# Kernel optimization log

Hardware: AMD Instinct MI355X
Metric: run time of the kernel (lower is better)

## Reference

```python
import jax, jax.numpy as jnp
import numpy as np

EPS = 0.01  # diffusion sampling noise scale


def gru_last(x, Wx, Wh, bx, bh):
    """Run a single-layer GRU (torch gate conventions) over x: [B, L, C] -> final hidden [B, H]."""
    B, L, C = x.shape
    H = Wh.shape[0]
    xg = jnp.einsum('blc,cg->blg', x, Wx) + bx  # precomputed input gates [B, L, 3H]

    def step(h, xg_t):
        hg = h @ Wh + bh
        xr, xz, xn = jnp.split(xg_t, 3, axis=-1)
        hr, hz, hn = jnp.split(hg, 3, axis=-1)
        r = jax.nn.sigmoid(xr + hr)
        z = jax.nn.sigmoid(xz + hz)
        n = jnp.tanh(xn + r * hn)
        h_new = (1.0 - z) * n + z * h
        return h_new, None

    h0 = jnp.zeros((B, H), x.dtype)
    h, _ = jax.lax.scan(step, h0, jnp.swapaxes(xg, 0, 1))
    return h


def gru_aggr(x, Wx, Wh, bx, bh, Wo, bo):
    return gru_last(x, Wx, Wh, bx, bh) @ Wo + bo


def setup_inputs() -> dict:
    key = jax.random.key(0)
    N, C, DEG, H, C_OUT, T = 8000, 64, 16, 128, 64, 4
    ks = jax.random.split(key, 16)

    def lin(k, fan_in, shape):
        return jax.random.normal(k, shape, dtype=jnp.float32) / np.sqrt(fan_in)

    inp = {
        'node_attr': jax.random.normal(ks[0], (N, C), dtype=jnp.float32),
        'neighbors': jax.random.randint(ks[1], (N, DEG), 0, N, dtype=jnp.int32),
        'noise': jax.random.normal(ks[2], (T, N, DEG), dtype=jnp.float32),
        # diff_aggr GRU + output head (edge log-prob comes from channel 0)
        'dWx': lin(ks[3], C, (C, 3 * H)),
        'dWh': lin(ks[4], H, (H, 3 * H)),
        'dbx': jnp.zeros((3 * H,), jnp.float32),
        'dbh': jnp.zeros((3 * H,), jnp.float32),
        'dWo': lin(ks[5], H, (H, C_OUT)),
        'dbo': jnp.zeros((C_OUT,), jnp.float32),
        # walk_aggr GRU + output head (node embedding)
        'wWx': lin(ks[6], C, (C, 3 * H)),
        'wWh': lin(ks[7], H, (H, 3 * H)),
        'wbx': jnp.zeros((3 * H,), jnp.float32),
        'wbh': jnp.zeros((3 * H,), jnp.float32),
        'wWo': lin(ks[8], H, (H, C_OUT)),
        'wbo': jnp.zeros((C_OUT,), jnp.float32),
    }
    return inp


def reference(node_attr, neighbors, noise,
              dWx, dWh, dbx, dbh, dWo, dbo,
              wWx, wWh, wbx, wbh, wWo, wbo):
    N, C = node_attr.shape
    DEG = neighbors.shape[1]
    T = noise.shape[0]

    cur = jnp.arange(N)                      # current frontier of each walk
    walk_embeds = node_attr[:, None, :]      # [N, L, C], L grows each step
    logps = []
    for t in range(T):
        nbr = neighbors[cur]                 # [N, DEG] candidate next hops
        cand = node_attr[nbr]                # [N, DEG, C]
        L = walk_embeds.shape[1]
        prefix = jnp.broadcast_to(walk_embeds[:, None], (N, DEG, L, C))
        seq = jnp.concatenate([prefix, cand[:, :, None, :]], axis=2)  # [N, DEG, L+1, C]
        seq = seq.reshape(N * DEG, L + 1, C)
        logp = gru_aggr(seq, dWx, dWh, dbx, dbh, dWo, dbo)[:, 0].reshape(N, DEG)
        # per-source-node log-softmax normalizer (no_grad in original)
        norm = jax.lax.stop_gradient(jax.nn.logsumexp(logp, axis=1, keepdims=True))
        logp = logp - norm
        p = jnp.exp(logp)
        noisy = p + EPS * noise[t]
        sel = jnp.argmax(noisy, axis=1)      # scatter_max over each node's candidates
        logps.append(jnp.take_along_axis(logp, sel[:, None], axis=1)[:, 0])
        cur = jnp.take_along_axis(nbr, sel[:, None], axis=1)[:, 0]
        walk_embeds = jnp.concatenate([walk_embeds, node_attr[cur][:, None, :]], axis=1)

    walks_logp = jnp.stack(logps, axis=1)    # [N, T]
    v_out = gru_aggr(walk_embeds, wWx, wWh, wbx, wbh, wWo, wbo)  # [N, C_OUT]
    return v_out, walks_logp
```

## Files before the change

### kernel.cpp

```cpp
#include <hip/hip_runtime.h>
#include <math.h>

#define NN 8000
#define CD 64
#define DG 16
#define HD 128
#define G3 384
#define TT 4
#define MARGIN 4e-3f

#if __has_builtin(__builtin_amdgcn_rcpf)
#define RCP(x) __builtin_amdgcn_rcpf(x)
#else
#define RCP(x) (1.f/(x))
#endif

__device__ __forceinline__ float fsig (float x){ return RCP(1.f + __expf(-x)); }
__device__ __forceinline__ float ftanh(float x){ return 1.f - 2.f*RCP(1.f + __expf(2.f*x)); }

__device__ __forceinline__ double fexp64(double x){
    const double LOG2E  = 1.4426950408889634074;
    const double LN2_HI = 6.93147180369123816490e-01;
    const double LN2_LO = 1.90821492927058770002e-10;
    x = fmin(fmax(x, -700.0), 700.0);
    double fn = rint(x * LOG2E);
    double r  = fma(-fn, LN2_HI, x);
    r = fma(-fn, LN2_LO, r);
    double p = 1.6059043836821613e-10;
    p = fma(p, r, 2.0876756987868099e-09);
    p = fma(p, r, 2.5052108385441719e-08);
    p = fma(p, r, 2.7557319223985893e-07);
    p = fma(p, r, 2.7557319223985888e-06);
    p = fma(p, r, 2.4801587301587302e-05);
    p = fma(p, r, 1.9841269841269841e-04);
    p = fma(p, r, 1.3888888888888889e-03);
    p = fma(p, r, 8.3333333333333332e-03);
    p = fma(p, r, 4.1666666666666664e-02);
    p = fma(p, r, 1.6666666666666666e-01);
    p = fma(p, r, 0.5);
    p = fma(p, r, 1.0);
    p = fma(p, r, 1.0);
    long long bits = __double_as_longlong(p) + ((long long)(int)fn << 52);
    return __longlong_as_double(bits);
}
__device__ __forceinline__ double sig64f (double x){ return 1.0/(1.0 + fexp64(-x)); }
__device__ __forceinline__ double tanh64f(double x){ return 1.0 - 2.0/(fexp64(2.0*x) + 1.0); }

__global__ __launch_bounds__(384) void xg_kernel(const float* __restrict__ A,
    const float* __restrict__ W, const float* __restrict__ b,
    float* __restrict__ hiP, float* __restrict__ loP)
{
    __shared__ float a_s[8][64];
    const int g  = threadIdx.x;
    const int l  = g & 63, q = g >> 6;
    const int n0 = blockIdx.x * 8;
    for (int idx = threadIdx.x; idx < 8*64; idx += 384)
        a_s[idx>>6][idx&63] = A[(size_t)n0*64 + idx];
    __syncthreads();
    double acc[8];
    const double bg = (double)b[g];
#pragma unroll
    for (int j=0;j<8;j++) acc[j] = bg;
    for (int c=0;c<64;c++){
        const double w = (double)W[c*G3 + g];
#pragma unroll
        for (int j=0;j<8;j++) acc[j] += (double)a_s[j][c]*w;
    }
#pragma unroll
    for (int j=0;j<8;j++){
        const size_t base = (size_t)(n0+j)*64 + l;
        const float hi = (float)acc[j];
        hiP[base*8 + q] = hi;
        if (q < 2) hiP[base*8 + 6 + q] = 0.f;
        if (loP) loP[base*6 + q] = (float)(acc[j] - (double)hi);
    }
}

__global__ __launch_bounds__(256) void repack_kernel(const float* __restrict__ W,
                                                     float* __restrict__ P)
{
    const int idx = blockIdx.x*256 + threadIdx.x;
    const int k = idx >> 9, rem = idx & 511, l = rem >> 3, s = rem & 7;
    P[idx] = (s < 6) ? W[k*G3 + s*64 + l] : 0.f;
}

__global__ __launch_bounds__(256) void walk_kernel(
    const int*   __restrict__ nbrs,  const float* __restrict__ noise,
    const float* __restrict__ XGfP,  const float* __restrict__ dWhP,
    const float* __restrict__ dbh,   const float* __restrict__ dWo,
    const float* __restrict__ dbo,
    int* __restrict__ paths, int* __restrict__ fail_cnt, int* __restrict__ fail_list,
    float* __restrict__ out)
{
    __shared__ float hf_s[4][HD];
    __shared__ float part_s[4][4][6][64];

    const int wid  = threadIdx.x >> 6;
    const int lane = threadIdx.x & 63;
    const int node = blockIdx.x*4 + wid;

    float h0 = 0.f, h1 = 0.f;
    float dbhf[6], hgf[6];
#pragma unroll
    for (int m=0;m<6;m++){ dbhf[m] = dbh[lane+64*m]; hgf[m] = dbhf[m]; }
    const float wo0f0 = dWo[lane*CD];
    const float wo0f1 = dWo[(lane+64)*CD];
    const float dbo0f = dbo[0];

    int cur = node;
    int ch0=0, ch1=0, ch2=0, ch3=0;
    int tripmask = 0;

    for (int t=0;t<TT;t++){
        if      (t==0) ch0 = cur;
        else if (t==1) ch1 = cur;
        else if (t==2) ch2 = cur;
        else           ch3 = cur;

        {
            const float4* xr = (const float4*)(XGfP + ((size_t)cur*64 + lane)*8);
            const float4 A = xr[0], B = xr[1];
            float r = fsig (A.x + hgf[0]);
            float z = fsig (A.z + hgf[2]);
            float n = ftanh(B.x + r*hgf[4]);
            h0 = (1.f-z)*n + z*h0;
            r = fsig (A.y + hgf[1]);
            z = fsig (A.w + hgf[3]);
            n = ftanh(B.y + r*hgf[5]);
            h1 = (1.f-z)*n + z*h1;
        }
        hf_s[wid][lane] = h0;  hf_s[wid][lane+64] = h1;
        __syncthreads();

        {
            float pacc[4][6];
#pragma unroll
            for (int j=0;j<4;j++)
#pragma unroll
                for (int m=0;m<6;m++) pacc[j][m] = 0.f;
            const float4* wr = (const float4*)(dWhP + (size_t)lane*8);
#pragma unroll 4
            for (int kk=0; kk<32; kk++){
                const int k = wid*32 + kk;
                const float4 W0 = wr[k*128], W1 = wr[k*128+1];
#pragma unroll
                for (int j=0;j<4;j++){
                    const float hk = hf_s[j][k];
                    pacc[j][0] += hk*W0.x; pacc[j][1] += hk*W0.y;
                    pacc[j][2] += hk*W0.z; pacc[j][3] += hk*W0.w;
                    pacc[j][4] += hk*W1.x; pacc[j][5] += hk*W1.y;
                }
            }
#pragma unroll
            for (int j=0;j<4;j++)
#pragma unroll
                for (int m=0;m<6;m++) part_s[wid][j][m][lane] = pacc[j][m];
        }
        __syncthreads();

#pragma unroll
        for (int m=0;m<6;m++)
            hgf[m] = dbhf[m] + part_s[0][wid][m][lane] + part_s[1][wid][m][lane]
                             + part_s[2][wid][m][lane] + part_s[3][wid][m][lane];

        int   nbrv = (lane < DG) ? nbrs[(size_t)cur*DG + lane] : 0;
        float nz   = (lane < DG) ? noise[((size_t)t*NN + node)*DG + lane] : 0.f;
        float lf = -3.0e38f;
#pragma unroll
        for (int g=0; g<4; g++){
            float4 CA[4], CB[4];
#pragma unroll
            for (int j=0;j<4;j++){
                const int nd = __shfl(nbrv, g*4+j);
                const float4* cr = (const float4*)(XGfP + ((size_t)nd*64 + lane)*8);
                CA[j] = cr[0];  CB[j] = cr[1];
            }
            float part[4];
#pragma unroll
            for (int j=0;j<4;j++){
                float r = fsig (CA[j].x + hgf[0]);
                float z = fsig (CA[j].z + hgf[2]);
                float n = ftanh(CB[j].x + r*hgf[4]);
                part[j]  = ((1.f-z)*n + z*h0) * wo0f0;
                r = fsig (CA[j].y + hgf[1]);
                z = fsig (CA[j].w + hgf[3]);
                n = ftanh(CB[j].y + r*hgf[5]);
                part[j] += ((1.f-z)*n + z*h1) * wo0f1;
            }
#pragma unroll
            for (int off=32; off>0; off>>=1){
#pragma unroll
                for (int j=0;j<4;j++) part[j] += __shfl_xor(part[j], off);
            }
#pragma unroll
            for (int j=0;j<4;j++) if (lane == g*4+j) lf = part[j] + dbo0f;
        }

        float v  = (lane < DG) ? lf : -3.0e38f;
        float mx = v;
#pragma unroll
        for (int off=32; off>0; off>>=1) mx = fmaxf(mx, __shfl_xor(mx, off));
        float e = (lane < DG) ? __expf(v - mx) : 0.f;
        float s = e;
#pragma unroll
        for (int off=32; off>0; off>>=1) s += __shfl_xor(s, off);
        const float normf = mx + __logf(s);

        float noisyf = (lane < DG) ? __expf(v - normf) + 0.01f*nz : -3.0e38f;
        int   idx = lane;
        float bv  = noisyf;
#pragma unroll
        for (int off=32; off>0; off>>=1){
            float ov = __shfl_xor(bv, off);
            int   oi = __shfl_xor(idx, off);
            if (ov > bv || (ov == bv && oi < idx)){ bv = ov; idx = oi; }
        }
        float sv = (lane == idx || lane >= DG) ? -3.0e38f : noisyf;
#pragma unroll
        for (int off=32; off>0; off>>=1) sv = fmaxf(sv, __shfl_xor(sv, off));

        if ((bv - sv) < MARGIN) tripmask |= (1 << t);

        const float lpf = __shfl(v, idx) - normf;
        if (lane == 0) out[NN*CD + node*TT + t] = lpf;
        cur = __shfl(nbrv, idx);
    }

    if (lane == 0){
        int* p = paths + (size_t)node*8;
        p[0]=ch0; p[1]=ch1; p[2]=ch2; p[3]=ch3; p[4]=cur;
        if (tripmask){
            const int slot = atomicAdd(fail_cnt, 1);
            if (slot < NN) fail_list[slot] = node | (tripmask << 16);
        }
    }
}

__global__ __launch_bounds__(256) void fix_kernel(
    const int*   __restrict__ nbrs,  const float* __restrict__ noise,
    const float* __restrict__ XGfP,  const float* __restrict__ XGrP,
    const float* __restrict__ dWhP,  const float* __restrict__ dbh,
    const float* __restrict__ dWo,   const float* __restrict__ dbo,
    const int* __restrict__ fail_cnt, const int* __restrict__ fail_list,
    int* __restrict__ paths, float* __restrict__ out)
{
    __shared__ double smem[3584];
    double* h_s  = smem;
    double* dbuf = smem + 512;

    const int wid  = threadIdx.x >> 6;
    const int lane = threadIdx.x & 63;
    const int count = min(fail_cnt[0], NN);
    if (blockIdx.x*4 >= count) return;

    const int  ii     = blockIdx.x*4 + wid;
    const bool active = (ii < count);
    const int  entry  = active ? fail_list[ii] : 0;
    const int  node   = entry & 0xFFFF;
    const int  mask   = active ? (entry >> 16) : 0;
    const int* pw     = paths + (size_t)node*8;

    double db64[6];
#pragma unroll
    for (int m=0;m<6;m++) db64[m] = (double)dbh[lane+64*m];
    const double wo0d0 = (double)dWo[lane*CD];
    const double wo0d1 = (double)dWo[(lane+64)*CD];
    const double dbo0d = (double)dbo[0];

    double H0 = 0.0, H1 = 0.0;
    double g64[6];
#pragma unroll
    for (int m=0;m<6;m++) g64[m] = db64[m];
    int  cur = node;
    int  c0=0,c1=0,c2=0,c3=0;
    bool diverged = false;

    for (int t=0;t<TT;t++){
        if      (t==0) c0 = cur;
        else if (t==1) c1 = cur;
        else if (t==2) c2 = cur;
        else           c3 = cur;

        {
            const size_t b = (size_t)cur*64 + lane;
            const float* hi = XGfP + b*8;
            const float* lo = XGrP + b*6;
            double r = sig64f (((double)hi[0]+(double)lo[0]) + g64[0]);
            double z = sig64f (((double)hi[2]+(double)lo[2]) + g64[2]);
            double n = tanh64f(((double)hi[4]+(double)lo[4]) + r*g64[4]);
            H0 = (1.0-z)*n + z*H0;
            r = sig64f (((double)hi[1]+(double)lo[1]) + g64[1]);
            z = sig64f (((double)hi[3]+(double)lo[3]) + g64[3]);
            n = tanh64f(((double)hi[5]+(double)lo[5]) + r*g64[5]);
            H1 = (1.0-z)*n + z*H1;
        }
        h_s[wid*HD + lane] = H0;  h_s[wid*HD + lane + 64] = H1;
        __syncthreads();

        double pacc[4][6];
#pragma unroll
        for (int j=0;j<4;j++)
#pragma unroll
            for (int m=0;m<6;m++) pacc[j][m] = 0.0;
        {
            const float4* wv = (const float4*)(dWhP + (size_t)lane*8);
#pragma unroll 4
            for (int kk=0; kk<32; kk++){
                const int k = wid*32 + kk;
                const float4 W0 = wv[k*128], W1 = wv[k*128+1];
#pragma unroll
                for (int j=0;j<4;j++){
                    const double hk = h_s[j*HD + k];
                    pacc[j][0] += hk*(double)W0.x; pacc[j][1] += hk*(double)W0.y;
                    pacc[j][2] += hk*(double)W0.z; pacc[j][3] += hk*(double)W0.w;
                    pacc[j][4] += hk*(double)W1.x; pacc[j][5] += hk*(double)W1.y;
                }
            }
        }
        if (wid >= 2){
#pragma unroll
            for (int j=0;j<4;j++)
#pragma unroll
                for (int m=0;m<6;m++)
                    dbuf[(((wid-2)*4+j)*6+m)*64 + lane] = pacc[j][m];
        }
        __syncthreads();
        if (wid < 2){
#pragma unroll
            for (int j=0;j<4;j++)
#pragma unroll
                for (int m=0;m<6;m++){
                    pacc[j][m] += dbuf[((wid*4+j)*6+m)*64 + lane];
                    dbuf[((wid*4+j)*6+m)*64 + lane] = pacc[j][m];
                }
        }
        __syncthreads();
#pragma unroll
        for (int m=0;m<6;m++)
            g64[m] = db64[m] + dbuf[((0*4+wid)*6+m)*64 + lane]
                             + dbuf[((1*4+wid)*6+m)*64 + lane];

        if (!diverged && !((mask >> t) & 1)){
            cur = pw[t+1];
            continue;
        }

        int   nbrv = (lane < DG) ? nbrs[(size_t)cur*DG + lane] : 0;
        float nz   = (lane < DG) ? noise[((size_t)t*NN + node)*DG + lane] : 0.f;
        double lv = -1e300;
#pragma unroll
        for (int g=0; g<4; g++){
            float ch[4][6], cl[4][6];
#pragma unroll
            for (int j=0;j<4;j++){
                const int nd = __shfl(nbrv, g*4+j);
                const size_t b = (size_t)nd*64 + lane;
                const float* hi = XGfP + b*8;
                const float* lo = XGrP + b*6;
#pragma unroll
                for (int q=0;q<6;q++){ ch[j][q]=hi[q]; cl[j][q]=lo[q]; }
            }
#pragma unroll
            for (int j=0;j<4;j++){
                double r = sig64f (((double)ch[j][0]+(double)cl[j][0]) + g64[0]);
                double z = sig64f (((double)ch[j][2]+(double)cl[j][2]) + g64[2]);
                double n = tanh64f(((double)ch[j][4]+(double)cl[j][4]) + r*g64[4]);
                double part = ((1.0-z)*n + z*H0) * wo0d0;
                r = sig64f (((double)ch[j][1]+(double)cl[j][1]) + g64[1]);
                z = sig64f (((double)ch[j][3]+(double)cl[j][3]) + g64[3]);
                n = tanh64f(((double)ch[j][5]+(double)cl[j][5]) + r*g64[5]);
                part += ((1.0-z)*n + z*H1) * wo0d1;
#pragma unroll
                for (int off=32; off>0; off>>=1) part += __shfl_xor(part, off);
                if (lane == g*4+j) lv = part + dbo0d;
            }
        }

        double dv = (lane < DG) ? lv : -1e300;
        double dmx = dv;
#pragma unroll
        for (int off=32; off>0; off>>=1) dmx = fmax(dmx, __shfl_xor(dmx, off));
        double de = (lane < DG) ? fexp64(dv - dmx) : 0.0;
        double ds = de;
#pragma unroll
        for (int off=32; off>0; off>>=1) ds += __shfl_xor(ds, off);
        const double dnorm = dmx + log(ds);
        double dnoisy = (lane < DG) ? fexp64(dv - dnorm) + 0.01*(double)nz : -1e300;
        int di = lane;
#pragma unroll
        for (int off=32; off>0; off>>=1){
            double ov = __shfl_xor(dnoisy, off);
            int    oi = __shfl_xor(di, off);
            if (ov > dnoisy || (ov == dnoisy && oi < di)){ dnoisy = ov; di = oi; }
        }
        const double lpfix = __shfl(dv, di) - dnorm;
        if (active && lane == 0) out[NN*CD + node*TT + t] = (float)lpfix;
        const int newcur = __shfl(nbrv, di);
        diverged = diverged || (newcur != pw[t+1]);
        cur = newcur;
    }

    if (active && lane == 0){
        int* p = paths + (size_t)node*8;
        p[0]=c0; p[1]=c1; p[2]=c2; p[3]=c3; p[4]=cur;
    }
}

__global__ __launch_bounds__(256) void wgru_kernel(
    const int*   __restrict__ paths, const float* __restrict__ XGwP,
    const float* __restrict__ wWhP,  const float* __restrict__ wbh,
    const float* __restrict__ wWo,   const float* __restrict__ wbo,
    float* __restrict__ out)
{
    __shared__ float hw_s[4][HD];
    __shared__ float part_s[4][4][6][64];
    const int wid  = threadIdx.x >> 6;
    const int lane = threadIdx.x & 63;
    const int node = blockIdx.x*4 + wid;

    float h0 = 0.f, h1 = 0.f;
    float wb[6], hg[6];
#pragma unroll
    for (int m=0;m<6;m++){ wb[m] = wbh[lane+64*m]; hg[m] = wb[m]; }
    const int* p = paths + (size_t)node*8;

#pragma unroll
    for (int s=0; s<=TT; s++){
        const int c = p[s];
        const float4* xr = (const float4*)(XGwP + ((size_t)c*64 + lane)*8);
        const float4 A = xr[0], B = xr[1];
        float r = fsig (A.x + hg[0]);
        float z = fsig (A.z + hg[2]);
        float n = ftanh(B.x + r*hg[4]);
        h0 = (1.f-z)*n + z*h0;
        r = fsig (A.y + hg[1]);
        z = fsig (A.w + hg[3]);
        n = ftanh(B.y + r*hg[5]);
        h1 = (1.f-z)*n + z*h1;
        if (s < TT){
            hw_s[wid][lane] = h0;  hw_s[wid][lane+64] = h1;
            __syncthreads();
            float pacc[4][6];
#pragma unroll
            for (int j=0;j<4;j++)
#pragma unroll
                for (int m=0;m<6;m++) pacc[j][m] = 0.f;
            const float4* wr = (const float4*)(wWhP + (size_t)lane*8);
#pragma unroll 4
            for (int kk=0; kk<32; kk++){
                const int k = wid*32 + kk;
                const float4 W0 = wr[k*128], W1 = wr[k*128+1];
#pragma unroll
                for (int j=0;j<4;j++){
                    const float hk = hw_s[j][k];
                    pacc[j][0] += hk*W0.x; pacc[j][1] += hk*W0.y;
                    pacc[j][2] += hk*W0.z; pacc[j][3] += hk*W0.w;
                    pacc[j][4] += hk*W1.x; pacc[j][5] += hk*W1.y;
                }
            }
#pragma unroll
            for (int j=0;j<4;j++)
#pragma unroll
                for (int m=0;m<6;m++) part_s[wid][j][m][lane] = pacc[j][m];
            __syncthreads();
#pragma unroll
            for (int m=0;m<6;m++)
                hg[m] = wb[m] + part_s[0][wid][m][lane] + part_s[1][wid][m][lane]
                              + part_s[2][wid][m][lane] + part_s[3][wid][m][lane];
        }
    }
    hw_s[wid][lane] = h0;  hw_s[wid][lane+64] = h1;
    __syncthreads();

    float acc = wbo[lane];
    const float* wcol = wWo + lane;
    for (int i=0;i<HD;i++) acc += hw_s[wid][i] * wcol[(size_t)i*CD];
    out[(size_t)node*CD + lane] = acc;
}

extern "C" void kernel_launch(void* const* d_in, const int* in_sizes, int n_in,
                              void* d_out, int out_size, void* d_ws, size_t ws_size,
                              hipStream_t stream)
{
    const float* attr  = (const float*)d_in[0];
    const int*   nbrs  = (const int*)  d_in[1];
    const float* noise = (const float*)d_in[2];
    const float* dWx = (const float*)d_in[3];
    const float* dWh = (const float*)d_in[4];
    const float* dbx = (const float*)d_in[5];
    const float* dbh = (const float*)d_in[6];
    const float* dWo = (const float*)d_in[7];
    const float* dbo = (const float*)d_in[8];
    const float* wWx = (const float*)d_in[9];
    const float* wWh = (const float*)d_in[10];
    const float* wbx = (const float*)d_in[11];
    const float* wbh = (const float*)d_in[12];
    const float* wWo = (const float*)d_in[13];
    const float* wbo = (const float*)d_in[14];
    float* out = (float*)d_out;

    char* ws = (char*)d_ws;
    float* XGfP      = (float*)(ws);
    float* XGrP      = (float*)(ws + 16384000);
    float* XGwP      = (float*)(ws + 28672000);
    float* dWhP      = (float*)(ws + 45056000);
    float* wWhP      = (float*)(ws + 45318144);
    int*   paths     = (int*)  (ws + 45580288);
    int*   fail_list = (int*)  (ws + 45836288);
    int*   fail_cnt  = (int*)  (ws + 45868288);

    hipMemsetAsync(fail_cnt, 0, sizeof(int), stream);

    xg_kernel<<<NN/8, G3, 0, stream>>>(attr, dWx, dbx, XGfP, XGrP);
    xg_kernel<<<NN/8, G3, 0, stream>>>(attr, wWx, wbx, XGwP, nullptr);
    repack_kernel<<<(HD*64*8)/256, 256, 0, stream>>>(dWh, dWhP);
    repack_kernel<<<(HD*64*8)/256, 256, 0, stream>>>(wWh, wWhP);

    walk_kernel<<<NN/4, 256, 0, stream>>>(nbrs, noise, XGfP, dWhP,
                                          dbh, dWo, dbo,
                                          paths, fail_cnt, fail_list, out);
    fix_kernel<<<2000, 256, 0, stream>>>(nbrs, noise, XGfP, XGrP,
                                         dWhP, dbh, dWo, dbo,
                                         fail_cnt, fail_list, paths, out);
    wgru_kernel<<<NN/4, 256, 0, stream>>>(paths, XGwP, wWhP, wbh, wWo, wbo, out);
}
```

Measured before the change: 525.3 us.

## Bin fix-list entries by last tripped step and exit fix blocks early

```diff
diff --git a/kernel.cpp b/kernel.cpp
--- a/kernel.cpp
+++ b/kernel.cpp
@@ -230,8 +230,9 @@
         int* p = paths + (size_t)node*8;
         p[0]=ch0; p[1]=ch1; p[2]=ch2; p[3]=ch3; p[4]=cur;
         if (tripmask){
-            const int slot = atomicAdd(fail_cnt, 1);
-            if (slot < NN) fail_list[slot] = node | (tripmask << 16);
+            const int bin = 31 - __clz(tripmask);
+            const int slot = atomicAdd(&fail_cnt[bin], 1);
+            fail_list[bin*NN + slot] = node | (tripmask << 16);
         }
     }
 }
@@ -250,15 +251,24 @@
 
     const int wid  = threadIdx.x >> 6;
     const int lane = threadIdx.x & 63;
-    const int count = min(fail_cnt[0], NN);
-    if (blockIdx.x*4 >= count) return;
+    const int n0c = fail_cnt[0], n1c = fail_cnt[1], n2c = fail_cnt[2], n3c = fail_cnt[3];
+    const int total = n0c + n1c + n2c + n3c;
+    if (blockIdx.x*4 >= total) return;
 
     const int  ii     = blockIdx.x*4 + wid;
-    const bool active = (ii < count);
-    const int  entry  = active ? fail_list[ii] : 0;
-    const int  node   = entry & 0xFFFF;
-    const int  mask   = active ? (entry >> 16) : 0;
-    const int* pw     = paths + (size_t)node*8;
+    const bool active = (ii < total);
+    int entry = 0;
+    if (active){
+        int b, loc;
+        if      (ii < n0c)            { b=0; loc=ii; }
+        else if (ii < n0c+n1c)        { b=1; loc=ii-n0c; }
+        else if (ii < n0c+n1c+n2c)    { b=2; loc=ii-n0c-n1c; }
+        else                          { b=3; loc=ii-n0c-n1c-n2c; }
+        entry = fail_list[b*NN + loc];
+    }
+    const int  node = entry & 0xFFFF;
+    const int  mask = active ? (entry >> 16) : 0;
+    const int* pw   = paths + (size_t)node*8;
 
     double db64[6];
 #pragma unroll
@@ -276,12 +286,15 @@
     bool diverged = false;
 
     for (int t=0;t<TT;t++){
+        const bool done = !diverged && ((mask >> t) == 0);
+        if (__syncthreads_and(done ? 1 : 0)) break;
+
         if      (t==0) c0 = cur;
         else if (t==1) c1 = cur;
         else if (t==2) c2 = cur;
         else           c3 = cur;
 
-        {
+        if (!done){
             const size_t b = (size_t)cur*64 + lane;
             const float* hi = XGfP + b*8;
             const float* lo = XGrP + b*6;
@@ -293,8 +306,8 @@
             z = sig64f (((double)hi[3]+(double)lo[3]) + g64[3]);
             n = tanh64f(((double)hi[5]+(double)lo[5]) + r*g64[5]);
             H1 = (1.0-z)*n + z*H1;
-        }
-        h_s[wid*HD + lane] = H0;  h_s[wid*HD + lane + 64] = H1;
+            h_s[wid*HD + lane] = H0;  h_s[wid*HD + lane + 64] = H1;
+        }
         __syncthreads();
 
         double pacc[4][6];
@@ -335,10 +348,12 @@
                 }
         }
         __syncthreads();
-#pragma unroll
-        for (int m=0;m<6;m++)
-            g64[m] = db64[m] + dbuf[((0*4+wid)*6+m)*64 + lane]
-                             + dbuf[((1*4+wid)*6+m)*64 + lane];
+        if (!done){
+#pragma unroll
+            for (int m=0;m<6;m++)
+                g64[m] = db64[m] + dbuf[((0*4+wid)*6+m)*64 + lane]
+                                 + dbuf[((1*4+wid)*6+m)*64 + lane];
+        }
 
         if (!diverged && !((mask >> t) & 1)){
             cur = pw[t+1];
@@ -400,7 +415,7 @@
         cur = newcur;
     }
 
-    if (active && lane == 0){
+    if (active && diverged && lane == 0){
         int* p = paths + (size_t)node*8;
         p[0]=c0; p[1]=c1; p[2]=c2; p[3]=c3; p[4]=cur;
     }
@@ -507,9 +522,9 @@
     float* wWhP      = (float*)(ws + 45318144);
     int*   paths     = (int*)  (ws + 45580288);
     int*   fail_list = (int*)  (ws + 45836288);
-    int*   fail_cnt  = (int*)  (ws + 45868288);
-
-    hipMemsetAsync(fail_cnt, 0, sizeof(int), stream);
+    int*   fail_cnt  = (int*)  (ws + 45964288);
+
+    hipMemsetAsync(fail_cnt, 0, 4*sizeof(int), stream);
 
     xg_kernel<<<NN/8, G3, 0, stream>>>(attr, dWx, dbx, XGfP, XGrP);
     xg_kernel<<<NN/8, G3, 0, stream>>>(attr, wWx, wbx, XGwP, nullptr);
```

New measurement: 492.9 us, median of 2. -6.2%, faster.
